# Optimization experiments

Hardware: AMD Instinct MI355X
Metric: run time of the kernel (lower is better)

The kernel has to match this reference:

```python
import jax, jax.numpy as jnp
import numpy as np

N_NODES = 100000
N_EDGES = 800000


def setup_inputs() -> dict:
    key = jax.random.key(0)
    ks = jax.random.split(key, 8)
    s = 0.05  # weight scale
    return {
        "x": jax.random.normal(ks[0], (N_NODES, 64), dtype=jnp.float32),
        "edge_index": jax.random.randint(ks[1], (2, N_EDGES), 0, N_NODES, dtype=jnp.int64),
        "eps1": jnp.zeros((), jnp.float32),
        "eps2": jnp.zeros((), jnp.float32),
        "W1a": jax.random.normal(ks[2], (64, 128), dtype=jnp.float32) * s,
        "b1a": jnp.zeros((128,), jnp.float32),
        "W1b": jax.random.normal(ks[3], (128, 128), dtype=jnp.float32) * s,
        "b1b": jnp.zeros((128,), jnp.float32),
        "W2a": jax.random.normal(ks[4], (128, 128), dtype=jnp.float32) * s,
        "b2a": jnp.zeros((128,), jnp.float32),
        "W2b": jax.random.normal(ks[5], (128, 64), dtype=jnp.float32) * s,
        "b2b": jnp.zeros((64,), jnp.float32),
    }


def _gin_conv(h, src, dst, eps, Wa, ba, Wb, bb, n_nodes):
    # sum-aggregate neighbor messages h[src] at dst, add (1+eps)*self
    agg = jax.ops.segment_sum(h[src], dst, num_segments=n_nodes)  # [N, d]
    z = (1.0 + eps) * h + agg
    # MLP: Linear -> ReLU -> Linear (weights stored [in, out])
    return jnp.maximum(z @ Wa + ba, 0.0) @ Wb + bb


def reference(x, edge_index, eps1, eps2, W1a, b1a, W1b, b1b, W2a, b2a, W2b, b2b):
    src, dst = edge_index[0], edge_index[1]
    n = x.shape[0]
    h = _gin_conv(x, src, dst, eps1, W1a, b1a, W1b, b1b, n)
    h = jnp.maximum(h, 0.0)  # outer ReLU; dropout is identity in eval
    out = _gin_conv(h, src, dst, eps2, W2a, b2a, W2b, b2b, n)
    return out
```

## Files before the change

### kernel.cpp

```cpp
#include <hip/hip_runtime.h>
#include <cstdint>

constexpr int CAP = 32;
constexpr int FIX = 16;

typedef __attribute__((ext_vector_type(8))) __bf16 bf16x8;
typedef __attribute__((ext_vector_type(16))) float f32x16;

__device__ __forceinline__ unsigned short f2bf(float f) {
    unsigned int u = __builtin_bit_cast(unsigned int, f);
    u += 0x7fffu + ((u >> 16) & 1u);
    return (unsigned short)(u >> 16);
}
__device__ __forceinline__ float bf2f(unsigned short h) {
    unsigned int u = ((unsigned int)h) << 16;
    return __builtin_bit_cast(float, u);
}


__global__ void init_kernel(int* __restrict__ counts, int N,
                            const float* __restrict__ W1a, const float* __restrict__ W1b,
                            const float* __restrict__ W2a, const float* __restrict__ W2b,
                            unsigned short* __restrict__ wpk,
                            const float* __restrict__ x, unsigned short* __restrict__ xbf) {
    int i = blockIdx.x * 256 + threadIdx.x;
    if (i < N) counts[i] = 0;
    if (i < 49152) {
        const float* W;
        int K, Nn, base, rel;
        if (i < 8192) {
            W = W1a; K = 64; Nn = 128; base = 0; rel = i;
        } else if (i < 24576) {
            W = W1b; K = 128; Nn = 128; base = 16384; rel = i - 8192;
        } else if (i < 40960) {
            W = W2a; K = 128; Nn = 128; base = 49152; rel = i - 24576;
        } else {
            W = W2b; K = 128; Nn = 64; base = 81920; rel = i - 40960;
        }
        int j = rel & 7;
        int lane = (rel >> 3) & 63;
        int rest = rel >> 9;
        int ksteps = K / 16;
        int kstep = rest % ksteps;
        int ntile = rest / ksteps;
        int k = kstep * 16 + ((lane >> 5) << 3) + j;
        int ncol = ntile * 32 + (lane & 31);
        float v = W[k * Nn + ncol];
        unsigned short h = f2bf(v);
        unsigned short l = f2bf(v - bf2f(h));
        wpk[base + rel] = h;
        wpk[base + K * Nn + rel] = l;
    }
    const int total4 = N * 16;
    const int stride = gridDim.x * 256;
    for (int t = i; t < total4; t += stride) {
        float4 v = ((const float4*)x)[t];
        ushort4 o;
        o.x = f2bf(v.x);
        o.y = f2bf(v.y);
        o.z = f2bf(v.z);
        o.w = f2bf(v.w);
        ((ushort4*)xbf)[t] = o;
    }
}


__global__ void bucket_kernel(const int* __restrict__ eidx, int E,
                              int* __restrict__ counts, int* __restrict__ buckets) {
    int e = blockIdx.x * 256 + threadIdx.x;
    if (e < E) {
        int d = eidx[E + e];
        int pos = atomicAdd(&counts[d], 1);
        if (pos < CAP) buckets[(size_t)d * CAP + pos] = eidx[e];
    }
}


template <int KIN, int KMID, int KOUT, bool RELU_OUT, bool SELF_F32, bool BF_OUT>
__global__ __launch_bounds__(512, 8) void gin_layer_kernel(
    const unsigned short* __restrict__ ghi, const unsigned short* __restrict__ glo,
    const float* __restrict__ hf32, const int* __restrict__ cnts,
    const int* __restrict__ buckets, const float* __restrict__ eps,
    const unsigned short* __restrict__ Wahi, const unsigned short* __restrict__ Walo,
    const float* __restrict__ ba,
    const unsigned short* __restrict__ Wbhi, const unsigned short* __restrict__ Wblo,
    const float* __restrict__ bb, float* __restrict__ out_f32,
    unsigned short* __restrict__ outhi, unsigned short* __restrict__ outlo, int n) {
    constexpr int ZS = KIN + 8;
    constexpr int TS = KMID + 8;
    constexpr int KSB = KIN / 16;
    constexpr int KSC = KMID / 16;
    __shared__ __align__(16) unsigned short smem[2 * 64 * (KMID + 8)];
    unsigned short* const zhi = smem;
    unsigned short* const zlo = smem + 64 * ZS;
    unsigned short* const thi = smem;
    unsigned short* const tlo = smem + 64 * TS;

    const int tid = threadIdx.x;
    const int lane = tid & 63;
    const int base = blockIdx.x * 64;
    const float scale = 1.0f + eps[0];
    const int wq = __builtin_amdgcn_readfirstlane(tid >> 6);

    float h0x, h0y;
    if (KIN == 64) {
        h0x = bf2f(ghi[lane]);
        h0y = 0.f;
    } else {
        unsigned int u0 = ((const unsigned int*)ghi)[lane];
        h0x = bf2f((unsigned short)(u0 & 0xffffu));
        h0y = bf2f((unsigned short)(u0 >> 16));
    }

#pragma unroll
    for (int mi = 0; mi < 8; ++mi) {
        const int m = wq * 8 + mi;
        const int node = base + m;
        const int nc = node < n ? node : n - 1;
        const int cl0 = __builtin_amdgcn_readfirstlane(cnts[nc]);
        const int cl = cl0 < CAP ? cl0 : CAP;
        const int* __restrict__ srcs = buckets + (size_t)nc * CAP;

        int sIdx[FIX];
#pragma unroll
        for (int j = 0; j < FIX; ++j) {
            int sj = srcs[j];
            sIdx[j] = j < cl ? sj : 0;
        }

        if (KIN == 64) {
            float a0 = 0.f, a1 = 0.f, a2 = 0.f, a3 = 0.f;
            float a4 = 0.f, a5 = 0.f, a6 = 0.f, a7 = 0.f;
#pragma unroll
            for (int j = 0; j < FIX; j += 8) {
                a0 += bf2f(ghi[(size_t)sIdx[j + 0] * 64 + lane]);
                a1 += bf2f(ghi[(size_t)sIdx[j + 1] * 64 + lane]);
                a2 += bf2f(ghi[(size_t)sIdx[j + 2] * 64 + lane]);
                a3 += bf2f(ghi[(size_t)sIdx[j + 3] * 64 + lane]);
                a4 += bf2f(ghi[(size_t)sIdx[j + 4] * 64 + lane]);
                a5 += bf2f(ghi[(size_t)sIdx[j + 5] * 64 + lane]);
                a6 += bf2f(ghi[(size_t)sIdx[j + 6] * 64 + lane]);
                a7 += bf2f(ghi[(size_t)sIdx[j + 7] * 64 + lane]);
            }
            float self;
            if (SELF_F32) {
                self = hf32[(size_t)nc * 64 + lane];
            } else {
                self = bf2f(ghi[(size_t)nc * 64 + lane]) + bf2f(glo[(size_t)nc * 64 + lane]);
            }
            float res = scale * self;
            res += ((a0 + a1) + (a2 + a3)) + ((a4 + a5) + (a6 + a7));
            float corr = (float)(FIX - (cl < FIX ? cl : FIX));
            res = __builtin_fmaf(-corr, h0x, res);
            for (int e = FIX; e < cl; ++e)
                res += bf2f(ghi[(size_t)srcs[e] * 64 + lane]);
            unsigned short rh = f2bf(res);
            zhi[m * ZS + lane] = rh;
            zlo[m * ZS + lane] = f2bf(res - bf2f(rh));
        } else {
            const unsigned int* g32 = (const unsigned int*)ghi;
            float x0 = 0.f, x1 = 0.f, x2 = 0.f, x3 = 0.f;
            float y0 = 0.f, y1 = 0.f, y2 = 0.f, y3 = 0.f;
#pragma unroll
            for (int j = 0; j < FIX; j += 4) {
                unsigned int v0 = g32[(size_t)sIdx[j + 0] * 64 + lane];
                unsigned int v1 = g32[(size_t)sIdx[j + 1] * 64 + lane];
                unsigned int v2 = g32[(size_t)sIdx[j + 2] * 64 + lane];
                unsigned int v3 = g32[(size_t)sIdx[j + 3] * 64 + lane];
                x0 += bf2f((unsigned short)(v0 & 0xffffu));
                y0 += bf2f((unsigned short)(v0 >> 16));
                x1 += bf2f((unsigned short)(v1 & 0xffffu));
                y1 += bf2f((unsigned short)(v1 >> 16));
                x2 += bf2f((unsigned short)(v2 & 0xffffu));
                y2 += bf2f((unsigned short)(v2 >> 16));
                x3 += bf2f((unsigned short)(v3 & 0xffffu));
                y3 += bf2f((unsigned short)(v3 >> 16));
            }
            float sx, sy;
            if (SELF_F32) {
                const float2* h2 = (const float2*)hf32;
                float2 a = h2[(size_t)nc * 64 + lane];
                sx = a.x;
                sy = a.y;
            } else {
                unsigned int sh = g32[(size_t)nc * 64 + lane];
                unsigned int sl = ((const unsigned int*)glo)[(size_t)nc * 64 + lane];
                sx = bf2f((unsigned short)(sh & 0xffffu)) + bf2f((unsigned short)(sl & 0xffffu));
                sy = bf2f((unsigned short)(sh >> 16)) + bf2f((unsigned short)(sl >> 16));
            }
            float ax = scale * sx + ((x0 + x1) + (x2 + x3));
            float ay = scale * sy + ((y0 + y1) + (y2 + y3));
            float corr = (float)(FIX - (cl < FIX ? cl : FIX));
            ax = __builtin_fmaf(-corr, h0x, ax);
            ay = __builtin_fmaf(-corr, h0y, ay);
            for (int e = FIX; e < cl; ++e) {
                unsigned int v = g32[(size_t)srcs[e] * 64 + lane];
                ax += bf2f((unsigned short)(v & 0xffffu));
                ay += bf2f((unsigned short)(v >> 16));
            }
            unsigned short hx = f2bf(ax), hy = f2bf(ay);
            unsigned short lx = f2bf(ax - bf2f(hx)), ly = f2bf(ay - bf2f(hy));
            *(unsigned int*)(zhi + m * ZS + 2 * lane) = (unsigned int)hx | ((unsigned int)hy << 16);
            *(unsigned int*)(zlo + m * ZS + 2 * lane) = (unsigned int)lx | ((unsigned int)ly << 16);
        }
    }
    __syncthreads();

    const int r31 = lane & 31;
    const int q = lane >> 5;

    {
        const int mt = wq & 1;
        const int nt = wq >> 1;
        f32x16 acc;
#pragma unroll
        for (int i = 0; i < 16; ++i) acc[i] = 0.0f;
        const unsigned short* Ah = zhi + (mt * 32 + r31) * ZS + q * 8;
        const unsigned short* Al = zlo + (mt * 32 + r31) * ZS + q * 8;
        const unsigned short* Bh = Wahi + ((size_t)(nt * KSB) * 64 + lane) * 8;
        const unsigned short* Bl = Walo + ((size_t)(nt * KSB) * 64 + lane) * 8;
#pragma unroll
        for (int ks = 0; ks < KSB; ++ks) {
            bf16x8 ah = *reinterpret_cast<const bf16x8*>(Ah + ks * 16);
            bf16x8 al = *reinterpret_cast<const bf16x8*>(Al + ks * 16);
            bf16x8 bh = *reinterpret_cast<const bf16x8*>(Bh + ks * 512);
            bf16x8 bl = *reinterpret_cast<const bf16x8*>(Bl + ks * 512);
            acc = __builtin_amdgcn_mfma_f32_32x32x16_bf16(ah, bh, acc, 0, 0, 0);
            acc = __builtin_amdgcn_mfma_f32_32x32x16_bf16(ah, bl, acc, 0, 0, 0);
            acc = __builtin_amdgcn_mfma_f32_32x32x16_bf16(al, bh, acc, 0, 0, 0);
        }
        const int col = nt * 32 + r31;
        const float bias = ba[col];
        unsigned short th_r[16], tl_r[16];
#pragma unroll
        for (int i = 0; i < 16; ++i) {
            float v = fmaxf(acc[i] + bias, 0.0f);
            unsigned short hh = f2bf(v);
            th_r[i] = hh;
            tl_r[i] = f2bf(v - bf2f(hh));
        }
        __syncthreads();
#pragma unroll
        for (int i = 0; i < 16; ++i) {
            const int m = mt * 32 + (i & 3) + 8 * (i >> 2) + 4 * q;
            thi[m * TS + col] = th_r[i];
            tlo[m * TS + col] = tl_r[i];
        }
    }
    __syncthreads();

    {
        constexpr int NKS = (KOUT == 64) ? (KSC / 2) : KSC;
        const int mt = wq & 1;
        const int nt = (KOUT == 64) ? ((wq >> 1) & 1) : (wq >> 1);
        const int k0 = (KOUT == 64) ? ((wq >> 2) * NKS) : 0;
        f32x16 acc;
#pragma unroll
        for (int i = 0; i < 16; ++i) acc[i] = 0.0f;
        const unsigned short* Ah = thi + (mt * 32 + r31) * TS + q * 8 + k0 * 16;
        const unsigned short* Al = tlo + (mt * 32 + r31) * TS + q * 8 + k0 * 16;
        const unsigned short* Bh = Wbhi + ((size_t)(nt * KSC + k0) * 64 + lane) * 8;
        const unsigned short* Bl = Wblo + ((size_t)(nt * KSC + k0) * 64 + lane) * 8;
#pragma unroll
        for (int ks = 0; ks < NKS; ++ks) {
            bf16x8 ah = *reinterpret_cast<const bf16x8*>(Ah + ks * 16);
            bf16x8 al = *reinterpret_cast<const bf16x8*>(Al + ks * 16);
            bf16x8 bh = *reinterpret_cast<const bf16x8*>(Bh + ks * 512);
            bf16x8 bl = *reinterpret_cast<const bf16x8*>(Bl + ks * 512);
            acc = __builtin_amdgcn_mfma_f32_32x32x16_bf16(ah, bh, acc, 0, 0, 0);
            acc = __builtin_amdgcn_mfma_f32_32x32x16_bf16(ah, bl, acc, 0, 0, 0);
            acc = __builtin_amdgcn_mfma_f32_32x32x16_bf16(al, bh, acc, 0, 0, 0);
        }
        const int col = nt * 32 + r31;
        if (KOUT == 64) {
            __syncthreads();
            float* stg = (float*)smem;
            if (wq >= 4) {
                float* d = stg + ((wq - 4) * 64 + lane) * 20;
#pragma unroll
                for (int c = 0; c < 4; ++c) {
                    float4 v = make_float4(acc[4 * c + 0], acc[4 * c + 1], acc[4 * c + 2],
                                           acc[4 * c + 3]);
                    *reinterpret_cast<float4*>(d + c * 4) = v;
                }
            }
            __syncthreads();
            if (wq < 4) {
                const float* s = stg + (wq * 64 + lane) * 20;
#pragma unroll
                for (int i = 0; i < 16; ++i) acc[i] += s[i];
                const float bias = bb[col];
#pragma unroll
                for (int i = 0; i < 16; ++i) {
                    const int m = mt * 32 + (i & 3) + 8 * (i >> 2) + 4 * q;
                    const int node = base + m;
                    if (node < n) {
                        float v = acc[i] + bias;
                        if (RELU_OUT) v = fmaxf(v, 0.0f);
                        out_f32[(size_t)node * KOUT + col] = v;
                    }
                }
            }
        } else {
            const float bias = bb[col];
#pragma unroll
            for (int i = 0; i < 16; ++i) {
                const int m = mt * 32 + (i & 3) + 8 * (i >> 2) + 4 * q;
                const int node = base + m;
                if (node < n) {
                    float v = acc[i] + bias;
                    if (RELU_OUT) v = fmaxf(v, 0.0f);
                    if (BF_OUT) {
                        unsigned short hh = f2bf(v);
                        outhi[(size_t)node * KOUT + col] = hh;
                        outlo[(size_t)node * KOUT + col] = f2bf(v - bf2f(hh));
                    } else {
                        out_f32[(size_t)node * KOUT + col] = v;
                    }
                }
            }
        }
    }
}


extern "C" void kernel_launch(void* const* d_in, const int* in_sizes, int n_in,
                              void* d_out, int out_size, void* d_ws, size_t ws_size,
                              hipStream_t stream) {
    const float* x = (const float*)d_in[0];
    const int* eidx = (const int*)d_in[1];
    const float* eps1 = (const float*)d_in[2];
    const float* eps2 = (const float*)d_in[3];
    const float* W1a = (const float*)d_in[4];
    const float* b1a = (const float*)d_in[5];
    const float* W1b = (const float*)d_in[6];
    const float* b1b = (const float*)d_in[7];
    const float* W2a = (const float*)d_in[8];
    const float* b2a = (const float*)d_in[9];
    const float* W2b = (const float*)d_in[10];
    const float* b2b = (const float*)d_in[11];
    float* out = (float*)d_out;

    int N = in_sizes[0] / 64;
    int E = in_sizes[1] / 2;

    char* p = (char*)d_ws;
    auto alloc = [&](size_t bytes) {
        char* r = p;
        p += (bytes + 255) & ~(size_t)255;
        return r;
    };
    int* counts = (int*)alloc((size_t)N * 4);
    int* buckets = (int*)alloc((size_t)N * CAP * 4);
    unsigned short* h1hi = (unsigned short*)alloc((size_t)N * 128 * 2);
    unsigned short* h1lo = (unsigned short*)alloc((size_t)N * 128 * 2);
    unsigned short* xbf = (unsigned short*)alloc((size_t)N * 64 * 2);
    unsigned short* wpk = (unsigned short*)alloc(98304 * 2);

    int ib = ((N > 49152 ? N : 49152) + 255) / 256;
    int eb = (E + 255) / 256;
    int gb = (N + 63) / 64;

    init_kernel<<<ib, 256, 0, stream>>>(counts, N, W1a, W1b, W2a, W2b, wpk, x, xbf);
    bucket_kernel<<<eb, 256, 0, stream>>>(eidx, E, counts, buckets);

    gin_layer_kernel<64, 128, 128, true, true, true><<<gb, 512, 0, stream>>>(
        xbf, (const unsigned short*)nullptr, x, counts, buckets, eps1, wpk + 0, wpk + 8192, b1a,
        wpk + 16384, wpk + 32768, b1b, (float*)nullptr, h1hi, h1lo, N);
    gin_layer_kernel<128, 128, 64, false, false, false><<<gb, 512, 0, stream>>>(
        h1hi, h1lo, (const float*)nullptr, counts, buckets, eps2, wpk + 49152, wpk + 65536, b2a,
        wpk + 81920, wpk + 90112, b2b, out, (unsigned short*)nullptr, (unsigned short*)nullptr, N);
}
```

Before: 246.2 us.

## Gather two nodes' neighbor rows at once to raise memory-level parallelism

The aggregation loop now processes node pairs, issuing all 32 neighbor gathers for both nodes before any accumulation, and preloads the eight per-wave edge counts up front. It also switches index arithmetic to 32-bit and uses cheaper bf16 unpack helpers. Launch bounds are relaxed from 8 to 4 blocks per CU so the extra in-flight loads have registers, which may lower occupancy.

```diff
diff --git a/kernel.cpp b/kernel.cpp
--- a/kernel.cpp
+++ b/kernel.cpp
@@ -15,6 +15,12 @@
 __device__ __forceinline__ float bf2f(unsigned short h) {
     unsigned int u = ((unsigned int)h) << 16;
     return __builtin_bit_cast(float, u);
+}
+__device__ __forceinline__ float bflo(unsigned int u) {
+    return __builtin_bit_cast(float, u << 16);
+}
+__device__ __forceinline__ float bfhi(unsigned int u) {
+    return __builtin_bit_cast(float, u & 0xffff0000u);
 }
 
 
@@ -77,7 +83,7 @@
 
 
 template <int KIN, int KMID, int KOUT, bool RELU_OUT, bool SELF_F32, bool BF_OUT>
-__global__ __launch_bounds__(512, 8) void gin_layer_kernel(
+__global__ __launch_bounds__(512, 4) void gin_layer_kernel(
     const unsigned short* __restrict__ ghi, const unsigned short* __restrict__ glo,
     const float* __restrict__ hf32, const int* __restrict__ cnts,
     const int* __restrict__ buckets, const float* __restrict__ eps,
@@ -108,100 +114,176 @@
         h0y = 0.f;
     } else {
         unsigned int u0 = ((const unsigned int*)ghi)[lane];
-        h0x = bf2f((unsigned short)(u0 & 0xffffu));
-        h0y = bf2f((unsigned short)(u0 >> 16));
-    }
-
-#pragma unroll
-    for (int mi = 0; mi < 8; ++mi) {
-        const int m = wq * 8 + mi;
-        const int node = base + m;
-        const int nc = node < n ? node : n - 1;
-        const int cl0 = __builtin_amdgcn_readfirstlane(cnts[nc]);
-        const int cl = cl0 < CAP ? cl0 : CAP;
-        const int* __restrict__ srcs = buckets + (size_t)nc * CAP;
-
-        int sIdx[FIX];
+        h0x = bflo(u0);
+        h0y = bfhi(u0);
+    }
+
+    const int nb0 = base + wq * 8;
+    int c8[8];
+    if (nb0 + 7 < n) {
+#pragma unroll
+        for (int i = 0; i < 8; ++i) c8[i] = cnts[nb0 + i];
+    } else {
+#pragma unroll
+        for (int i = 0; i < 8; ++i) c8[i] = (nb0 + i) < n ? cnts[nb0 + i] : 0;
+    }
+#pragma unroll
+    for (int i = 0; i < 8; ++i) c8[i] = c8[i] < CAP ? c8[i] : CAP;
+
+#pragma unroll
+    for (int mp = 0; mp < 8; mp += 2) {
+        const int mA = wq * 8 + mp;
+        const int mB = mA + 1;
+        const int ncA = (base + mA) < n ? (base + mA) : n - 1;
+        const int ncB = (base + mB) < n ? (base + mB) : n - 1;
+        const int clA = c8[mp];
+        const int clB = c8[mp + 1];
+        const int* __restrict__ srcsA = buckets + (size_t)ncA * CAP;
+        const int* __restrict__ srcsB = buckets + (size_t)ncB * CAP;
+
+        unsigned int iA[FIX], iB[FIX];
 #pragma unroll
         for (int j = 0; j < FIX; ++j) {
-            int sj = srcs[j];
-            sIdx[j] = j < cl ? sj : 0;
+            int t = srcsA[j];
+            iA[j] = (unsigned int)(j < clA ? t : 0);
+        }
+#pragma unroll
+        for (int j = 0; j < FIX; ++j) {
+            int t = srcsB[j];
+            iB[j] = (unsigned int)(j < clB ? t : 0);
         }
 
         if (KIN == 64) {
-            float a0 = 0.f, a1 = 0.f, a2 = 0.f, a3 = 0.f;
-            float a4 = 0.f, a5 = 0.f, a6 = 0.f, a7 = 0.f;
-#pragma unroll
-            for (int j = 0; j < FIX; j += 8) {
-                a0 += bf2f(ghi[(size_t)sIdx[j + 0] * 64 + lane]);
-                a1 += bf2f(ghi[(size_t)sIdx[j + 1] * 64 + lane]);
-                a2 += bf2f(ghi[(size_t)sIdx[j + 2] * 64 + lane]);
-                a3 += bf2f(ghi[(size_t)sIdx[j + 3] * 64 + lane]);
-                a4 += bf2f(ghi[(size_t)sIdx[j + 4] * 64 + lane]);
-                a5 += bf2f(ghi[(size_t)sIdx[j + 5] * 64 + lane]);
-                a6 += bf2f(ghi[(size_t)sIdx[j + 6] * 64 + lane]);
-                a7 += bf2f(ghi[(size_t)sIdx[j + 7] * 64 + lane]);
-            }
-            float self;
+            unsigned short vA[FIX], vB[FIX];
+#pragma unroll
+            for (int j = 0; j < FIX; ++j) vA[j] = ghi[iA[j] * 64u + lane];
+#pragma unroll
+            for (int j = 0; j < FIX; ++j) vB[j] = ghi[iB[j] * 64u + lane];
+            float selfA, selfB;
             if (SELF_F32) {
-                self = hf32[(size_t)nc * 64 + lane];
+                selfA = hf32[(unsigned int)ncA * 64u + lane];
+                selfB = hf32[(unsigned int)ncB * 64u + lane];
             } else {
-                self = bf2f(ghi[(size_t)nc * 64 + lane]) + bf2f(glo[(size_t)nc * 64 + lane]);
-            }
-            float res = scale * self;
-            res += ((a0 + a1) + (a2 + a3)) + ((a4 + a5) + (a6 + a7));
-            float corr = (float)(FIX - (cl < FIX ? cl : FIX));
-            res = __builtin_fmaf(-corr, h0x, res);
-            for (int e = FIX; e < cl; ++e)
-                res += bf2f(ghi[(size_t)srcs[e] * 64 + lane]);
-            unsigned short rh = f2bf(res);
-            zhi[m * ZS + lane] = rh;
-            zlo[m * ZS + lane] = f2bf(res - bf2f(rh));
+                selfA = bf2f(ghi[(unsigned int)ncA * 64u + lane]) +
+                        bf2f(glo[(unsigned int)ncA * 64u + lane]);
+                selfB = bf2f(ghi[(unsigned int)ncB * 64u + lane]) +
+                        bf2f(glo[(unsigned int)ncB * 64u + lane]);
+            }
+            {
+                float s0 = 0.f, s1 = 0.f, s2 = 0.f, s3 = 0.f;
+#pragma unroll
+                for (int j = 0; j < FIX; j += 4) {
+                    s0 += bf2f(vA[j + 0]);
+                    s1 += bf2f(vA[j + 1]);
+                    s2 += bf2f(vA[j + 2]);
+                    s3 += bf2f(vA[j + 3]);
+                }
+                float res = scale * selfA + ((s0 + s1) + (s2 + s3));
+                float corr = (float)(FIX - (clA < FIX ? clA : FIX));
+                res = __builtin_fmaf(-corr, h0x, res);
+                for (int e = FIX; e < clA; ++e)
+                    res += bf2f(ghi[(unsigned int)srcsA[e] * 64u + lane]);
+                unsigned short rh = f2bf(res);
+                zhi[mA * ZS + lane] = rh;
+                zlo[mA * ZS + lane] = f2bf(res - bf2f(rh));
+            }
+            {
+                float s0 = 0.f, s1 = 0.f, s2 = 0.f, s3 = 0.f;
+#pragma unroll
+                for (int j = 0; j < FIX; j += 4) {
+                    s0 += bf2f(vB[j + 0]);
+                    s1 += bf2f(vB[j + 1]);
+                    s2 += bf2f(vB[j + 2]);
+                    s3 += bf2f(vB[j + 3]);
+                }
+                float res = scale * selfB + ((s0 + s1) + (s2 + s3));
+                float corr = (float)(FIX - (clB < FIX ? clB : FIX));
+                res = __builtin_fmaf(-corr, h0x, res);
+                for (int e = FIX; e < clB; ++e)
+                    res += bf2f(ghi[(unsigned int)srcsB[e] * 64u + lane]);
+                unsigned short rh = f2bf(res);
+                zhi[mB * ZS + lane] = rh;
+                zlo[mB * ZS + lane] = f2bf(res - bf2f(rh));
+            }
         } else {
             const unsigned int* g32 = (const unsigned int*)ghi;
-            float x0 = 0.f, x1 = 0.f, x2 = 0.f, x3 = 0.f;
-            float y0 = 0.f, y1 = 0.f, y2 = 0.f, y3 = 0.f;
-#pragma unroll
-            for (int j = 0; j < FIX; j += 4) {
-                unsigned int v0 = g32[(size_t)sIdx[j + 0] * 64 + lane];
-                unsigned int v1 = g32[(size_t)sIdx[j + 1] * 64 + lane];
-                unsigned int v2 = g32[(size_t)sIdx[j + 2] * 64 + lane];
-                unsigned int v3 = g32[(size_t)sIdx[j + 3] * 64 + lane];
-                x0 += bf2f((unsigned short)(v0 & 0xffffu));
-                y0 += bf2f((unsigned short)(v0 >> 16));
-                x1 += bf2f((unsigned short)(v1 & 0xffffu));
-                y1 += bf2f((unsigned short)(v1 >> 16));
-                x2 += bf2f((unsigned short)(v2 & 0xffffu));
-                y2 += bf2f((unsigned short)(v2 >> 16));
-                x3 += bf2f((unsigned short)(v3 & 0xffffu));
-                y3 += bf2f((unsigned short)(v3 >> 16));
-            }
-            float sx, sy;
+            unsigned int vA[FIX], vB[FIX];
+#pragma unroll
+            for (int j = 0; j < FIX; ++j) vA[j] = g32[iA[j] * 64u + lane];
+#pragma unroll
+            for (int j = 0; j < FIX; ++j) vB[j] = g32[iB[j] * 64u + lane];
+            float sxA, syA, sxB, syB;
             if (SELF_F32) {
                 const float2* h2 = (const float2*)hf32;
-                float2 a = h2[(size_t)nc * 64 + lane];
-                sx = a.x;
-                sy = a.y;
+                float2 a = h2[(unsigned int)ncA * 64u + lane];
+                sxA = a.x;
+                syA = a.y;
+                float2 b = h2[(unsigned int)ncB * 64u + lane];
+                sxB = b.x;
+                syB = b.y;
             } else {
-                unsigned int sh = g32[(size_t)nc * 64 + lane];
-                unsigned int sl = ((const unsigned int*)glo)[(size_t)nc * 64 + lane];
-                sx = bf2f((unsigned short)(sh & 0xffffu)) + bf2f((unsigned short)(sl & 0xffffu));
-                sy = bf2f((unsigned short)(sh >> 16)) + bf2f((unsigned short)(sl >> 16));
-            }
-            float ax = scale * sx + ((x0 + x1) + (x2 + x3));
-            float ay = scale * sy + ((y0 + y1) + (y2 + y3));
-            float corr = (float)(FIX - (cl < FIX ? cl : FIX));
-            ax = __builtin_fmaf(-corr, h0x, ax);
-            ay = __builtin_fmaf(-corr, h0y, ay);
-            for (int e = FIX; e < cl; ++e) {
-                unsigned int v = g32[(size_t)srcs[e] * 64 + lane];
-                ax += bf2f((unsigned short)(v & 0xffffu));
-                ay += bf2f((unsigned short)(v >> 16));
-            }
-            unsigned short hx = f2bf(ax), hy = f2bf(ay);
-            unsigned short lx = f2bf(ax - bf2f(hx)), ly = f2bf(ay - bf2f(hy));
-            *(unsigned int*)(zhi + m * ZS + 2 * lane) = (unsigned int)hx | ((unsigned int)hy << 16);
-            *(unsigned int*)(zlo + m * ZS + 2 * lane) = (unsigned int)lx | ((unsigned int)ly << 16);
+                const unsigned int* l32 = (const unsigned int*)glo;
+                unsigned int shA = g32[(unsigned int)ncA * 64u + lane];
+                unsigned int slA = l32[(unsigned int)ncA * 64u + lane];
+                sxA = bflo(shA) + bflo(slA);
+                syA = bfhi(shA) + bfhi(slA);
+                unsigned int shB = g32[(unsigned int)ncB * 64u + lane];
+                unsigned int slB = l32[(unsigned int)ncB * 64u + lane];
+                sxB = bflo(shB) + bflo(slB);
+                syB = bfhi(shB) + bfhi(slB);
+            }
+            {
+                float x0 = 0.f, x1 = 0.f, y0 = 0.f, y1 = 0.f;
+#pragma unroll
+                for (int j = 0; j < FIX; j += 2) {
+                    x0 += bflo(vA[j]);
+                    y0 += bfhi(vA[j]);
+                    x1 += bflo(vA[j + 1]);
+                    y1 += bfhi(vA[j + 1]);
+                }
+                float ax = scale * sxA + (x0 + x1);
+                float ay = scale * syA + (y0 + y1);
+                float corr = (float)(FIX - (clA < FIX ? clA : FIX));
+                ax = __builtin_fmaf(-corr, h0x, ax);
+                ay = __builtin_fmaf(-corr, h0y, ay);
+                for (int e = FIX; e < clA; ++e) {
+                    unsigned int v = g32[(unsigned int)srcsA[e] * 64u + lane];
+                    ax += bflo(v);
+                    ay += bfhi(v);
+                }
+                unsigned short hx = f2bf(ax), hy = f2bf(ay);
+                unsigned short lx = f2bf(ax - bf2f(hx)), ly = f2bf(ay - bf2f(hy));
+                *(unsigned int*)(zhi + mA * ZS + 2 * lane) =
+                    (unsigned int)hx | ((unsigned int)hy << 16);
+                *(unsigned int*)(zlo + mA * ZS + 2 * lane) =
+                    (unsigned int)lx | ((unsigned int)ly << 16);
+            }
+            {
+                float x0 = 0.f, x1 = 0.f, y0 = 0.f, y1 = 0.f;
+#pragma unroll
+                for (int j = 0; j < FIX; j += 2) {
+                    x0 += bflo(vB[j]);
+                    y0 += bfhi(vB[j]);
+                    x1 += bflo(vB[j + 1]);
+                    y1 += bfhi(vB[j + 1]);
+                }
+                float ax = scale * sxB + (x0 + x1);
+                float ay = scale * syB + (y0 + y1);
+                float corr = (float)(FIX - (clB < FIX ? clB : FIX));
+                ax = __builtin_fmaf(-corr, h0x, ax);
+                ay = __builtin_fmaf(-corr, h0y, ay);
+                for (int e = FIX; e < clB; ++e) {
+                    unsigned int v = g32[(unsigned int)srcsB[e] * 64u + lane];
+                    ax += bflo(v);
+                    ay += bfhi(v);
+                }
+                unsigned short hx = f2bf(ax), hy = f2bf(ay);
+                unsigned short lx = f2bf(ax - bf2f(hx)), ly = f2bf(ay - bf2f(hy));
+                *(unsigned int*)(zhi + mB * ZS + 2 * lane) =
+                    (unsigned int)hx | ((unsigned int)hy << 16);
+                *(unsigned int*)(zlo + mB * ZS + 2 * lane) =
+                    (unsigned int)lx | ((unsigned int)ly << 16);
+            }
         }
     }
     __syncthreads();
```

New measurement: 252.2 us. 2.5% more time.
